# Kernel tuning notes

Measured on AMD Instinct MI355X. Metric: run time of the kernel, lower is better.

The kernel has to match this reference:

```python
import jax, jax.numpy as jnp
import numpy as np

RATIO = 0.5  # SAGPooling ratio


def setup_inputs() -> dict:
    key = jax.random.key(0)
    ks = jax.random.split(key, 6)
    B, n, d, out_dim, Eg = 128, 512, 256, 256, 4096  # graphs, nodes/graph, feat, proj out, edges/graph
    N = B * n
    x = jax.random.normal(ks[0], (N, d), dtype=jnp.float32)
    # edges connect nodes within the same graph (contiguous node blocks)
    src = jax.random.randint(ks[1], (B, Eg), 0, n)
    dst = jax.random.randint(ks[2], (B, Eg), 0, n)
    off = (jnp.arange(B) * n)[:, None]
    edge_index = jnp.stack([(src + off).reshape(-1), (dst + off).reshape(-1)]).astype(jnp.int32)
    batch = jnp.repeat(jnp.arange(B), n).astype(jnp.int32)
    s = 1.0 / np.sqrt(d).astype(np.float32)
    w_rel = jax.random.normal(ks[3], (d, 1), dtype=jnp.float32) * s   # GraphConv lin_rel (has bias)
    b_rel = jnp.zeros((1,), dtype=jnp.float32)
    w_root = jax.random.normal(ks[4], (d, 1), dtype=jnp.float32) * s  # GraphConv lin_root (no bias)
    w_proj = jax.random.normal(ks[5], (d, out_dim), dtype=jnp.float32) * s  # projection Linear
    b_proj = jnp.zeros((out_dim,), dtype=jnp.float32)
    return {"x": x, "edge_index": edge_index, "batch": batch, "num_graphs": B,
            "w_rel": w_rel, "b_rel": b_rel, "w_root": w_root,
            "w_proj": w_proj, "b_proj": b_proj}


def reference(x, edge_index, batch, num_graphs, w_rel, b_rel, w_root, w_proj, b_proj):
    N, d = x.shape
    n = N // num_graphs                    # equal-size graphs
    k = int(np.ceil(RATIO * n))            # PyG topk: ceil(ratio * num_nodes)
    src, dst = edge_index[0], edge_index[1]
    # GraphConv(node_dim, 1): score_i = lin_rel(sum_{j->i} x_j) + lin_root(x_i)
    agg = jax.ops.segment_sum(x[src], dst, num_segments=N)          # [N, d]
    score = jnp.tanh((agg @ w_rel + b_rel + x @ w_root)[:, 0])       # [N], tanh nonlinearity
    sb = score.reshape(num_graphs, n)                                # [B, n]
    top_vals, top_idx = jax.lax.top_k(sb, k)                         # per-graph topk
    xb = x.reshape(num_graphs, n, d)
    x_sel = jnp.take_along_axis(xb, top_idx[:, :, None], axis=1)     # [B, k, d]
    x_sel = x_sel * top_vals[:, :, None]                             # x[perm] * score[perm] (multiplier=1)
    pooled = x_sel.mean(axis=1)                                      # global_mean_pool over k kept nodes
    return pooled @ w_proj + b_proj                                  # [B, out_dim]
```

## Files before the change

### kernel.cpp

```cpp
#include <hip/hip_runtime.h>

#define D        256
#define NPG      512
#define BG       128
#define KSEL     256
#define EPG      4096
#define NN       (BG * NPG)
#define ET       (BG * EPG)

__global__ __launch_bounds__(256) void k_proj_scores(
        const float* __restrict__ x,
        const float* __restrict__ w_rel, const float* __restrict__ w_root,
        float* __restrict__ p, float* __restrict__ r) {
    int tid  = threadIdx.x;
    int wave = tid >> 6, lane = tid & 63;
    int node = blockIdx.x * 4 + wave;

    const float4* x4  = (const float4*)(x + (size_t)node * D);
    float4 xv = x4[lane];
    float4 wr = ((const float4*)w_rel)[lane];
    float4 wo = ((const float4*)w_root)[lane];
    float pv = xv.x * wr.x + xv.y * wr.y + xv.z * wr.z + xv.w * wr.w;
    float rv = xv.x * wo.x + xv.y * wo.y + xv.z * wo.z + xv.w * wo.w;
    #pragma unroll
    for (int off = 32; off; off >>= 1) {
        pv += __shfl_xor(pv, off, 64);
        rv += __shfl_xor(rv, off, 64);
    }
    if (lane == 0) { p[node] = pv; r[node] = rv; }
}

__global__ __launch_bounds__(1024) void k_select_pool(
        const float* __restrict__ x, const int* __restrict__ ei,
        const float* __restrict__ p, const float* __restrict__ r,
        const float* __restrict__ b_rel,
        float* __restrict__ ppart) {
    __shared__ __align__(16) float s_p[NPG];
    __shared__ __align__(16) float s_agg[NPG];
    __shared__ __align__(16) float s_val[NPG];
    __shared__ int   s_cnt4[1024];
    __shared__ int   s_selid[256];
    __shared__ __align__(16) float s_selv[256];
    __shared__ __align__(16) float s_red[16][D];
    __shared__ int   s_nsel;

    int blk = blockIdx.x;
    int b = blk >> 1, half = blk & 1;
    int tid = threadIdx.x, wave = tid >> 6, lane = tid & 63;
    int base = b * NPG;

    if (tid < NPG) { s_p[tid] = p[base + tid]; s_agg[tid] = 0.f; }
    if (tid == 0)  s_nsel = 0;
    __syncthreads();

    {
        const int* src = ei + (size_t)b * EPG;
        const int* dst = ei + ET + (size_t)b * EPG;
        #pragma unroll
        for (int e = tid; e < EPG; e += 1024)
            atomicAdd(&s_agg[dst[e] - base], s_p[src[e] - base]);
    }
    __syncthreads();

    if (tid < NPG)
        s_val[tid] = tanhf(s_agg[tid] + b_rel[0] + r[base + tid]);
    __syncthreads();

    {
        int j = half * 256 + (tid & 255);
        int q = tid >> 8;
        float sv = s_val[j];
        const float4* v4 = (const float4*)s_val + q * 32;
        int i0b = q * 128;
        int c = 0;
        #pragma unroll 8
        for (int t = 0; t < 32; ++t) {
            float4 o = v4[t];
            int i0 = i0b + t * 4;
            c += (o.x > sv) || (o.x == sv && (i0 + 0) < j);
            c += (o.y > sv) || (o.y == sv && (i0 + 1) < j);
            c += (o.z > sv) || (o.z == sv && (i0 + 2) < j);
            c += (o.w > sv) || (o.w == sv && (i0 + 3) < j);
        }
        s_cnt4[tid] = c;
    }
    __syncthreads();
    if (tid < 256) {
        int rank = s_cnt4[tid] + s_cnt4[tid + 256] + s_cnt4[tid + 512] + s_cnt4[tid + 768];
        if (rank < KSEL) {
            int pos = atomicAdd(&s_nsel, 1);
            s_selid[pos] = half * 256 + tid;
            s_selv[pos]  = s_val[half * 256 + tid];
        }
    }
    __syncthreads();
    int nsel = s_nsel;

    {
        float4 acc = {0.f, 0.f, 0.f, 0.f};
        for (int s = wave; s < nsel; s += 16) {
            int row = s_selid[s];
            float v = s_selv[s];
            float4 xv = ((const float4*)(x + (size_t)(base + row) * D))[lane];
            acc.x += v * xv.x; acc.y += v * xv.y;
            acc.z += v * xv.z; acc.w += v * xv.w;
        }
        ((float4*)s_red[wave])[lane] = acc;
    }
    __syncthreads();

    if (tid < D) {
        float s = 0.f;
        #pragma unroll
        for (int w = 0; w < 16; ++w) s += s_red[w][tid];
        ppart[(size_t)blk * D + tid] = s;
    }
}

__global__ __launch_bounds__(1024) void k_project(
        const float* __restrict__ ppart,
        const float* __restrict__ w_proj, const float* __restrict__ b_proj,
        float* __restrict__ out) {
    __shared__ __align__(16) float s_pool[D];
    __shared__ __align__(16) float s_red[4][D];
    int b = blockIdx.x, tid = threadIdx.x;
    if (tid < D)
        s_pool[tid] = ppart[(size_t)(2 * b) * D + tid]
                    + ppart[(size_t)(2 * b + 1) * D + tid];
    __syncthreads();
    {
        int f = tid & (D - 1);
        int q = tid >> 8;
        const float4* pool4 = (const float4*)s_pool + q * 16;
        const float* wp = w_proj + (size_t)(q * 64) * D + f;
        float acc = 0.f;
        #pragma unroll
        for (int t = 0; t < 16; ++t) {
            float4 pv = pool4[t];
            acc += pv.x * wp[(t * 4 + 0) * D];
            acc += pv.y * wp[(t * 4 + 1) * D];
            acc += pv.z * wp[(t * 4 + 2) * D];
            acc += pv.w * wp[(t * 4 + 3) * D];
        }
        s_red[q][f] = acc;
    }
    __syncthreads();
    if (tid < D)
        out[(size_t)b * D + tid] = b_proj[tid] +
            (s_red[0][tid] + s_red[1][tid] + s_red[2][tid] + s_red[3][tid]) * (1.0f / KSEL);
}

extern "C" void kernel_launch(void* const* d_in, const int* in_sizes, int n_in,
                              void* d_out, int out_size, void* d_ws, size_t ws_size,
                              hipStream_t stream) {
    const float* x      = (const float*)d_in[0];
    const int*   ei     = (const int*)d_in[1];
    const float* w_rel  = (const float*)d_in[4];
    const float* b_rel  = (const float*)d_in[5];
    const float* w_root = (const float*)d_in[6];
    const float* w_proj = (const float*)d_in[7];
    const float* b_proj = (const float*)d_in[8];
    float* out = (float*)d_out;

    float* p     = (float*)d_ws;
    float* r     = p + NN;
    float* ppart = r + NN;

    k_proj_scores<<<NN / 4, 256, 0, stream>>>(x, w_rel, w_root, p, r);
    k_select_pool<<<2 * BG, 1024, 0, stream>>>(x, ei, p, r, b_rel, ppart);
    k_project<<<BG, 1024, 0, stream>>>(ppart, w_proj, b_proj, out);
}
```

Measured before the change: 128.2 us.

## Replace all-pairs rank counting with radix-histogram top-k selection

Per-graph top-k selection changes from an O(n^2) pairwise comparison count to an 8-bit radix histogram on order-preserving float keys. A wave-level suffix scan finds the threshold bin, and only nodes in that bin are ranked pairwise. Ranking runs on the pre-tanh score, with tanh applied only to selected nodes, which relies on tanh being monotonic. It adds more barriers and shared memory, and many scores may fall into one bin, which would make the candidate ranking loop long and serial.

```diff
diff --git a/kernel.cpp b/kernel.cpp
--- a/kernel.cpp
+++ b/kernel.cpp
@@ -30,6 +30,11 @@
     if (lane == 0) { p[node] = pv; r[node] = rv; }
 }
 
+__device__ inline unsigned sortkey(float s) {
+    unsigned u = __float_as_uint(s);
+    return u ^ (unsigned)(((int)u >> 31) | 0x80000000);
+}
+
 __global__ __launch_bounds__(1024) void k_select_pool(
         const float* __restrict__ x, const int* __restrict__ ei,
         const float* __restrict__ p, const float* __restrict__ r,
@@ -38,11 +43,15 @@
     __shared__ __align__(16) float s_p[NPG];
     __shared__ __align__(16) float s_agg[NPG];
     __shared__ __align__(16) float s_val[NPG];
-    __shared__ int   s_cnt4[1024];
-    __shared__ int   s_selid[256];
+    __shared__ unsigned s_key[NPG];
+    __shared__ int      s_sel[NPG];
+    __shared__ int      s_hist[256];
+    __shared__ unsigned s_candkey[NPG];
+    __shared__ int      s_candidx[NPG];
+    __shared__ int      s_selid[256];
     __shared__ __align__(16) float s_selv[256];
     __shared__ __align__(16) float s_red[16][D];
-    __shared__ int   s_nsel;
+    __shared__ int s_nsel, s_ncand, s_B, s_m;
 
     int blk = blockIdx.x;
     int b = blk >> 1, half = blk & 1;
@@ -50,7 +59,12 @@
     int base = b * NPG;
 
     if (tid < NPG) { s_p[tid] = p[base + tid]; s_agg[tid] = 0.f; }
-    if (tid == 0)  s_nsel = 0;
+    else {
+        int j = tid - NPG;
+        s_sel[j] = 0;
+        if (j < 256) s_hist[j] = 0;
+    }
+    if (tid == 0) { s_nsel = 0; s_ncand = 0; }
     __syncthreads();
 
     {
@@ -62,35 +76,82 @@
     }
     __syncthreads();
 
-    if (tid < NPG)
-        s_val[tid] = tanhf(s_agg[tid] + b_rel[0] + r[base + tid]);
-    __syncthreads();
-
-    {
-        int j = half * 256 + (tid & 255);
-        int q = tid >> 8;
-        float sv = s_val[j];
-        const float4* v4 = (const float4*)s_val + q * 32;
-        int i0b = q * 128;
-        int c = 0;
-        #pragma unroll 8
-        for (int t = 0; t < 32; ++t) {
-            float4 o = v4[t];
-            int i0 = i0b + t * 4;
-            c += (o.x > sv) || (o.x == sv && (i0 + 0) < j);
-            c += (o.y > sv) || (o.y == sv && (i0 + 1) < j);
-            c += (o.z > sv) || (o.z == sv && (i0 + 2) < j);
-            c += (o.w > sv) || (o.w == sv && (i0 + 3) < j);
-        }
-        s_cnt4[tid] = c;
-    }
-    __syncthreads();
+    if (tid < NPG) {
+        float s = s_agg[tid] + b_rel[0] + r[base + tid];
+        s_val[tid] = s;
+        unsigned k = sortkey(s);
+        s_key[tid] = k;
+        atomicAdd(&s_hist[k >> 24], 1);
+    }
+    __syncthreads();
+
+    if (wave == 0) {
+        int c0 = s_hist[4 * lane + 0], c1 = s_hist[4 * lane + 1];
+        int c2 = s_hist[4 * lane + 2], c3 = s_hist[4 * lane + 3];
+        int lsum = c0 + c1 + c2 + c3;
+        int suf = lsum;
+        #pragma unroll
+        for (int off = 1; off < 64; off <<= 1) {
+            int v = __shfl_down(suf, off, 64);
+            if (lane + off < 64) suf += v;
+        }
+        int above = suf - lsum;
+        int a3 = above, a2 = a3 + c3, a1 = a2 + c2, a0 = a1 + c1;
+        if (a3 < KSEL && KSEL <= a3 + c3) { s_B = 4 * lane + 3; s_m = a3; }
+        if (a2 < KSEL && KSEL <= a2 + c2) { s_B = 4 * lane + 2; s_m = a2; }
+        if (a1 < KSEL && KSEL <= a1 + c1) { s_B = 4 * lane + 1; s_m = a1; }
+        if (a0 < KSEL && KSEL <= a0 + c0) { s_B = 4 * lane + 0; s_m = a0; }
+    }
+    __syncthreads();
+    int B = s_B, kk = KSEL - s_m;
+
+    {
+        int cand = 0;
+        if (tid < NPG) {
+            int bin = s_key[tid] >> 24;
+            if (bin > B) s_sel[tid] = 1;
+            cand = (bin == B);
+        }
+        unsigned long long mball = __ballot(cand);
+        if (mball) {
+            int wbase = 0;
+            if (lane == 0) wbase = atomicAdd(&s_ncand, __popcll(mball));
+            wbase = __shfl(wbase, 0, 64);
+            if (cand) {
+                int pos = wbase + __popcll(mball & ((1ull << lane) - 1ull));
+                s_candkey[pos] = s_key[tid];
+                s_candidx[pos] = tid;
+            }
+        }
+    }
+    __syncthreads();
+    int ncand = s_ncand;
+
+    if (tid < ncand) {
+        unsigned mykey = s_candkey[tid];
+        int myidx = s_candidx[tid];
+        int rnk = 0;
+        for (int i = 0; i < ncand; ++i) {
+            unsigned ok = s_candkey[i];
+            rnk += (ok > mykey) || (ok == mykey && s_candidx[i] < myidx);
+        }
+        if (rnk < kk) s_sel[myidx] = 1;
+    }
+    __syncthreads();
+
     if (tid < 256) {
-        int rank = s_cnt4[tid] + s_cnt4[tid + 256] + s_cnt4[tid + 512] + s_cnt4[tid + 768];
-        if (rank < KSEL) {
-            int pos = atomicAdd(&s_nsel, 1);
-            s_selid[pos] = half * 256 + tid;
-            s_selv[pos]  = s_val[half * 256 + tid];
+        int node = half * 256 + tid;
+        int sel = s_sel[node];
+        unsigned long long mball = __ballot(sel);
+        if (mball) {
+            int wbase = 0;
+            if (lane == 0) wbase = atomicAdd(&s_nsel, __popcll(mball));
+            wbase = __shfl(wbase, 0, 64);
+            if (sel) {
+                int pos = wbase + __popcll(mball & ((1ull << lane) - 1ull));
+                s_selid[pos] = node;
+                s_selv[pos]  = tanhf(s_val[node]);
+            }
         }
     }
     __syncthreads();
```

After: 133.7 us. +4.3%, slower.
